# Kernel optimization log

Measured on AMD Instinct MI355X. Metric: run time of the kernel, lower is better.

The kernel has to match this reference:

```python
import jax, jax.numpy as jnp
import numpy as np

DIM = 192; HEADS = 6; WIN = 8; HIDDEN = int(DIM * 2.66); EPS = 1e-5

def dct_matrix(n):
    # DCT-II orthonormal matrix, matches get_dctMatrix(n, n)
    i = np.arange(n)[:, None]; j = np.arange(n)[None, :]
    M = np.cos(np.pi * i * (2 * j + 1) / (2 * n)) * np.sqrt(2.0 / n)
    M[0, :] = np.sqrt(1.0 / n)
    return jnp.asarray(M, dtype=jnp.float32)

def layernorm_c(x, w, b):
    # WithBias LayerNorm over channel dim of BCHW (restormer to_3d/to_4d style)
    mu = x.mean(axis=1, keepdims=True)
    var = ((x - mu) ** 2).mean(axis=1, keepdims=True)
    return (x - mu) / jnp.sqrt(var + EPS) * w[None, :, None, None] + b[None, :, None, None]

def conv1x1(x, w, b=None):
    y = jnp.einsum('oc,bchw->bohw', w, x)
    return y if b is None else y + b[None, :, None, None]

def dwconv3x3(x, w):
    return jax.lax.conv_general_dilated(x, w, (1, 1), ((1, 1), (1, 1)),
        dimension_numbers=('NCHW', 'OIHW', 'NCHW'), feature_group_count=x.shape[1])

def l2norm(x):
    n = jnp.sqrt(jnp.sum(x * x, axis=-1, keepdims=True))
    return x / jnp.maximum(n, 1e-12)

def window_channel_attn(qkv, temperature):
    # 'b (z head c) (h1 h) (w1 w) -> z (b h1 w1) head c (h w)'
    b, _, H, W = qkv.shape
    cph = DIM // HEADS
    h1, w1 = H // WIN, W // WIN
    t = qkv.reshape(b, 3, HEADS, cph, h1, WIN, w1, WIN)
    t = t.transpose(1, 0, 4, 6, 2, 3, 5, 7).reshape(3, b * h1 * w1, HEADS, cph, WIN * WIN)
    q, k, v = t[0], t[1], t[2]
    q = l2norm(q); k = l2norm(k)
    attn = jnp.einsum('nhce,nhde->nhcd', q, k) * temperature[None]  # channel x channel per window
    attn = jax.nn.softmax(attn, axis=-1)
    out = jnp.einsum('nhcd,nhde->nhce', attn, v)
    out = out.reshape(b, h1, w1, HEADS, cph, WIN, WIN)
    out = out.transpose(0, 3, 4, 1, 5, 2, 6).reshape(b, DIM, H, W)
    return out

def forward(x, norm1_w, norm1_b, w_qkv, w_dw, temperature, w_proj, b_proj,
            norm2_w, norm2_b, w_in, w_dwf, w_out):
    B, C, H, W = x.shape
    Mh = dct_matrix(H); Mw = dct_matrix(W)
    # attention branch in DCT domain
    y = layernorm_c(x, norm1_w, norm1_b)
    y = jnp.einsum('ph,bchw->bcpw', Mh, y)      # dct2dx: Mh @ y @ Mw.T
    y = jnp.einsum('bcpw,qw->bcpq', y, Mw)
    qkv = dwconv3x3(conv1x1(y, w_qkv), w_dw)
    a = window_channel_attn(qkv, temperature)
    a = conv1x1(a, w_proj, b_proj)
    a = jnp.einsum('bcpq,qw->bcpw', a, Mw)      # idct2dx: Mh.T @ a @ Mw
    a = jnp.einsum('bcpw,ph->bchw', a, Mh)
    x1 = x + a
    # gated-dconv FFN branch
    z = layernorm_c(x1, norm2_w, norm2_b)
    f = dwconv3x3(conv1x1(z, w_in), w_dwf)
    f1, f2 = jnp.split(f, 2, axis=1)
    f = jax.nn.gelu(f1, approximate=False) * f2
    f = conv1x1(f, w_out)
    return x1 + f

def setup_inputs() -> dict:
    key = jax.random.key(0)
    ks = jax.random.split(key, 8)
    B, C, H, W = 2, DIM, 192, 192
    s = 0.02
    return {
        'x': jax.random.normal(ks[0], (B, C, H, W), jnp.float32),
        'norm1_w': jnp.ones((C,), jnp.float32),
        'norm1_b': jnp.zeros((C,), jnp.float32),
        'w_qkv': jax.random.normal(ks[1], (3 * C, C), jnp.float32) * s,
        'w_dw': jax.random.normal(ks[2], (3 * C, 1, 3, 3), jnp.float32) * s,
        'temperature': jnp.ones((HEADS, 1, 1), jnp.float32) / np.float32(np.sqrt(C)),
        'w_proj': jax.random.normal(ks[3], (C, C), jnp.float32) * s,
        'b_proj': jnp.zeros((C,), jnp.float32),
        'norm2_w': jnp.ones((C,), jnp.float32),
        'norm2_b': jnp.zeros((C,), jnp.float32),
        'w_in': jax.random.normal(ks[4], (2 * HIDDEN, C), jnp.float32) * s,
        'w_dwf': jax.random.normal(ks[5], (2 * HIDDEN, 1, 3, 3), jnp.float32) * s,
        'w_out': jax.random.normal(ks[6], (C, HIDDEN), jnp.float32) * s,
    }

def reference(x, norm1_w, norm1_b, w_qkv, w_dw, temperature, w_proj, b_proj,
              norm2_w, norm2_b, w_in, w_dwf, w_out):
    return forward(x, norm1_w, norm1_b, w_qkv, w_dw, temperature, w_proj, b_proj,
                   norm2_w, norm2_b, w_in, w_dwf, w_out)
```

## Files before the change

kernel.cpp:

```cpp
#include <hip/hip_runtime.h>
#include <hip/hip_bf16.h>

typedef __hip_bfloat16 bft;
typedef __attribute__((ext_vector_type(8))) short bf16x8;
typedef __attribute__((ext_vector_type(4))) float f32x4;

#define BLK 256
static constexpr int Cc = 192;
static constexpr int L  = 192;
static constexpr int S  = 36864;
static constexpr int Bn = 2;
static constexpr int HID = 510;
static constexpr int CH = 64;
static constexpr int FTR = (CH + 2) * L;
static constexpr int GTR = CH * L;
static constexpr double PI_D = 3.141592653589793238462643383279502884;

__device__ __forceinline__ float ldf(const float* p) { return *p; }
__device__ __forceinline__ float ldf(const bft* p)   { return __bfloat162float(*p); }
__device__ __forceinline__ void  stf(float* p, float v) { *p = v; }
__device__ __forceinline__ void  stf(bft* p, float v)   { *p = __float2bfloat16(v); }
__device__ __forceinline__ unsigned short f2bfu(float f) {
    bft h = __float2bfloat16(f);
    return *reinterpret_cast<const unsigned short*>(&h);
}
__device__ __forceinline__ unsigned short bfu(const bft* p) {
    return *reinterpret_cast<const unsigned short*>(p);
}
__device__ __forceinline__ float bu2f(unsigned short u) {
    unsigned int x = (unsigned int)u << 16;
    return __uint_as_float(x);
}
__device__ __forceinline__ bf16x8 ld8(const unsigned short* p) {
    union { unsigned int u[4]; bf16x8 v; } t;
    const unsigned int* q = reinterpret_cast<const unsigned int*>(p);
    t.u[0] = q[0]; t.u[1] = q[1]; t.u[2] = q[2]; t.u[3] = q[3];
    return t.v;
}

__global__ __launch_bounds__(BLK) void k_dct_init(bft* __restrict__ dctb,
                                                  bft* __restrict__ dctTb) {
    int idx = blockIdx.x * BLK + threadIdx.x;
    if (idx >= L * L) return;
    int p = idx / L, h = idx - p * L;
    double v = (p == 0) ? sqrt(1.0 / L)
                        : cos(PI_D * p * (2 * h + 1) / (2.0 * L)) * sqrt(2.0 / L);
    bft bv = __float2bfloat16((float)v);
    dctb[p * L + h] = bv;
    dctTb[h * L + p] = bv;
}

__global__ __launch_bounds__(BLK) void k_cvt(const float* __restrict__ src,
                                             bft* __restrict__ dst,
                                             int Mr, int Kr, int Kp) {
    int idx = blockIdx.x * BLK + threadIdx.x;
    int m = idx / Kp, k = idx - m * Kp;
    float v = (m < Mr && k < Kr) ? src[(size_t)m * Kr + k] : 0.f;
    dst[idx] = __float2bfloat16(v);
}

__global__ __launch_bounds__(BLK) void k_cvt_ffn(const float* __restrict__ src,
                                                 bft* __restrict__ dst) {
    int idx = blockIdx.x * BLK + threadIdx.x;
    int m = idx / Cc, k = idx - m * Cc;
    float v = 0.f;
    if (m < 510) v = src[(size_t)m * Cc + k];
    else if (m >= 512 && m < 1022) v = src[(size_t)(m - 2) * Cc + k];
    dst[idx] = __float2bfloat16(v);
}

template <typename TI, bool TRANS>
__global__ __launch_bounds__(BLK) void k_lnt(const TI* __restrict__ x,
                                             const float* __restrict__ w,
                                             const float* __restrict__ b,
                                             bft* __restrict__ out,
                                             long zI, long zO) {
    __shared__ float t[192][65];
    __shared__ float mus[64], rs[64];
    const int tid = threadIdx.x;
    const int s0 = blockIdx.x * 64;
    const TI* xp = x + (size_t)blockIdx.y * zI;
    if constexpr (sizeof(TI) == 4) {
        for (int id = tid; id < 192 * 16; id += BLK) {
            int c = id >> 4, q = id & 15;
            float4 v = *reinterpret_cast<const float4*>(
                (const float*)xp + (size_t)c * S + s0 + q * 4);
            t[c][q * 4 + 0] = v.x; t[c][q * 4 + 1] = v.y;
            t[c][q * 4 + 2] = v.z; t[c][q * 4 + 3] = v.w;
        }
    } else {
        for (int id = tid; id < 192 * 8; id += BLK) {
            int c = id >> 3, q = id & 7;
            uint4 raw = *reinterpret_cast<const uint4*>(
                (const bft*)xp + (size_t)c * S + s0 + q * 8);
            const unsigned short* u = reinterpret_cast<const unsigned short*>(&raw);
#pragma unroll
            for (int e = 0; e < 8; ++e) t[c][q * 8 + e] = bu2f(u[e]);
        }
    }
    __syncthreads();
    {
        int px = tid >> 2, g = tid & 3;
        float sum = 0.f, sq = 0.f;
#pragma unroll
        for (int j = 0; j < 48; ++j) {
            float v = t[g * 48 + j][px];
            sum += v; sq += v * v;
        }
        sum += __shfl_xor(sum, 1); sum += __shfl_xor(sum, 2);
        sq  += __shfl_xor(sq, 1);  sq  += __shfl_xor(sq, 2);
        float mu = sum * (1.f / Cc);
        float var = sq * (1.f / Cc) - mu * mu;
        float r = rsqrtf(var + 1e-5f);
        if (g == 0) { mus[px] = mu; rs[px] = r; }
    }
    __syncthreads();
    bft* op = out + (size_t)blockIdx.y * zO;
    if constexpr (!TRANS) {
        for (int id = tid; id < 192 * 8; id += BLK) {
            int c = id >> 3, q = id & 7;
            float wc = w[c], bc = b[c];
            unsigned short v8[8];
#pragma unroll
            for (int e = 0; e < 8; ++e) {
                int px = q * 8 + e;
                v8[e] = f2bfu((t[c][px] - mus[px]) * rs[px] * wc + bc);
            }
            *reinterpret_cast<uint4*>(op + (size_t)c * S + s0 + q * 8) =
                *reinterpret_cast<uint4*>(v8);
        }
    } else {
#pragma unroll
        for (int qq = 0; qq < 3; ++qq) {
            for (int id = tid; id < 512; id += BLK) {
                int s = id >> 3, qlo = id & 7;
                int q = qq * 8 + qlo;
                float mu = mus[s], r = rs[s];
                unsigned short v8[8];
#pragma unroll
                for (int e = 0; e < 8; ++e) {
                    int c = q * 8 + e;
                    v8[e] = f2bfu((t[c][s] - mu) * r * w[c] + b[c]);
                }
                *reinterpret_cast<uint4*>(op + (size_t)(s0 + s) * Cc + q * 8) =
                    *reinterpret_cast<uint4*>(v8);
            }
        }
    }
}

__global__ __launch_bounds__(BLK) void k_tr(const bft* __restrict__ in,
                                            bft* __restrict__ out, long z) {
    __shared__ unsigned short t[32][72];
    const int tid = threadIdx.x;
    const int s0 = blockIdx.x * 64, c0 = blockIdx.y * 32;
    const bft* ip = in + (size_t)blockIdx.z * z;
    bft* op = out + (size_t)blockIdx.z * z;
    {
        int c = tid >> 3, sc = (tid & 7) * 8;
        *reinterpret_cast<uint4*>(&t[c][sc]) =
            *reinterpret_cast<const uint4*>(ip + (size_t)(c0 + c) * S + s0 + sc);
    }
    __syncthreads();
    {
        int s = tid >> 2, cc = (tid & 3) * 8;
        unsigned short v[8];
#pragma unroll
        for (int q = 0; q < 8; ++q) v[q] = t[cc + q][s];
        *reinterpret_cast<uint4*>(op + (size_t)(s0 + s) * Cc + c0 + cc) =
            *reinterpret_cast<uint4*>(v);
    }
}

__global__ __launch_bounds__(BLK) void k_w2s(const bft* __restrict__ src,
                                             bft* __restrict__ dst,
                                             long zI, long zO) {
    __shared__ unsigned short t[192][100];
    const int tid = threadIdx.x;
    const int hh = blockIdx.x;
    const int ch0 = blockIdx.y * 96;
    const int bz = blockIdx.z;
    const int h1 = hh >> 3, ii = hh & 7;
    const bft* ip = src + (size_t)bz * zI;
    for (int id = tid; id < 192 * 12; id += BLK) {
        int r = id / 12, q = id - r * 12;
        int w1 = r >> 3, jj = r & 7;
        int s = (h1 * 24 + w1) * 64 + ii * 8 + jj;
        *reinterpret_cast<uint4*>(&t[r][q * 8]) =
            *reinterpret_cast<const uint4*>(ip + (size_t)s * Cc + ch0 + q * 8);
    }
    __syncthreads();
    bft* op = dst + (size_t)bz * zO;
    for (int id = tid; id < 96 * 24; id += BLK) {
        int c = id / 24, q = id - c * 24;
        unsigned short v[8];
#pragma unroll
        for (int e = 0; e < 8; ++e) v[e] = t[q * 8 + e][c];
        *reinterpret_cast<uint4*>(op + (size_t)(ch0 + c) * S + (size_t)hh * L + q * 8) =
            *reinterpret_cast<uint4*>(v);
    }
}

template <int WR, int WC, int FM, int FN, int KSTEP, int BMODE, int OMODE,
          bool GSWAP, bool SWIZ, bool AMASK, bool HASBIAS, bool BIASN,
          bool HASRES, typename OutT, typename ResT>
__global__ __launch_bounds__(256) void k_mm(
    const bft* __restrict__ A, int strideA, int Mreal, long zA,
    const bft* __restrict__ B, int strideB, long zB,
    OutT* __restrict__ Out, int strideO, long zO,
    const float* __restrict__ bias,
    const ResT* __restrict__ Res, long zR,
    int K, int rlo, int rhi) {
    constexpr int BM = WR * FM * 16, BN = WC * FN * 16;
    constexpr int AV = KSTEP / 8;
    constexpr int KL = (BM + BN) * (KSTEP + 8);
    constexpr int RST = (OMODE == 3) ? BN * (BM + 8)
                      : (OMODE == 5 ? BM * (BN + 8) : 0);
    constexpr int LDSZ = (KL > RST) ? KL : RST;
    __shared__ unsigned short lds[LDSZ];
    unsigned short (*Al)[KSTEP + 8] =
        reinterpret_cast<unsigned short(*)[KSTEP + 8]>(lds);
    unsigned short (*Bl)[KSTEP + 8] =
        reinterpret_cast<unsigned short(*)[KSTEP + 8]>(lds + BM * (KSTEP + 8));
    const int tid = threadIdx.x;
    int bx = blockIdx.x, by = blockIdx.y;
    if constexpr (SWIZ) {
        int nbx = gridDim.x, nby = gridDim.y;
        int nwg = nbx * nby;
        int orig = bx + nbx * by;
        int cpx = nwg >> 3;
        int swz = (orig & 7) * cpx + (orig >> 3);
        bx = swz % nbx; by = swz / nbx;
    }
    const int n0 = (GSWAP ? by : bx) * BN;
    const int m0 = (GSWAP ? bx : by) * BM;
    const int bz = blockIdx.z;
    const int lane = tid & 63, wv = tid >> 6;
    const int wr = wv / WC, wc = wv % WC;
    const int l15 = lane & 15, l4 = lane >> 4;
    f32x4 acc[FM][FN] = {};

    const bft* Ab = A + (size_t)bz * zA;
    const bft* Bb = B + (size_t)bz * zB;

    for (int k0 = 0; k0 < K; k0 += KSTEP) {
        for (int id = tid; id < BM * AV; id += 256) {
            int row = id / AV, kc = (id % AV) * 8;
            int gm = m0 + row;
            if constexpr (AMASK) {
                uint4 val = make_uint4(0, 0, 0, 0);
                if (gm >= rlo && gm < rhi)
                    val = *reinterpret_cast<const uint4*>(
                        Ab + (size_t)gm * strideA + k0 + kc);
                *reinterpret_cast<uint4*>(&Al[row][kc]) = val;
            } else {
                if (gm >= Mreal) gm = Mreal - 1;
                *reinterpret_cast<uint4*>(&Al[row][kc]) =
                    *reinterpret_cast<const uint4*>(Ab + (size_t)gm * strideA + k0 + kc);
            }
        }
        for (int id = tid; id < BN * AV; id += 256) {
            int row = id / AV, kc = (id % AV) * 8;
            int gn = n0 + row;
            uint4 val;
            if constexpr (BMODE == 2) {
                val = *reinterpret_cast<const uint4*>(
                    Bb + (size_t)gn * strideB + k0 + kc);
            } else {
                if (gn >= rlo && gn < rhi)
                    val = *reinterpret_cast<const uint4*>(
                        Bb + (size_t)gn * strideB + k0 + kc);
                else
                    val = make_uint4(0, 0, 0, 0);
            }
            *reinterpret_cast<uint4*>(&Bl[row][kc]) = val;
        }
        __syncthreads();
#pragma unroll
        for (int kk = 0; kk < KSTEP / 32; ++kk) {
            bf16x8 af[FM], bf[FN];
#pragma unroll
            for (int i = 0; i < FM; ++i)
                af[i] = *reinterpret_cast<const bf16x8*>(
                    &Al[wr * FM * 16 + i * 16 + l15][kk * 32 + l4 * 8]);
#pragma unroll
            for (int j = 0; j < FN; ++j)
                bf[j] = *reinterpret_cast<const bf16x8*>(
                    &Bl[wc * FN * 16 + j * 16 + l15][kk * 32 + l4 * 8]);
#pragma unroll
            for (int i = 0; i < FM; ++i)
#pragma unroll
                for (int j = 0; j < FN; ++j)
                    acc[i][j] = __builtin_amdgcn_mfma_f32_16x16x32_bf16(
                        af[i], bf[j], acc[i][j], 0, 0, 0);
        }
        __syncthreads();
    }
    if constexpr (OMODE == 3) {
        constexpr int OST = BM + 8;
        unsigned short* Ol = lds;
#pragma unroll
        for (int i = 0; i < FM; ++i) {
            int mB = wr * FM * 16 + i * 16 + l4 * 4;
#pragma unroll
            for (int j = 0; j < FN; ++j) {
                int n = wc * FN * 16 + j * 16 + l15;
                unsigned short v[4];
#pragma unroll
                for (int r = 0; r < 4; ++r) v[r] = f2bfu(acc[i][j][r]);
                *reinterpret_cast<uint2*>(&Ol[n * OST + mB]) =
                    *reinterpret_cast<uint2*>(v);
            }
        }
        __syncthreads();
        constexpr int TPR = BM / 64;
        for (int row = tid / TPR; row < BN; row += 256 / TPR) {
            int seg = (tid % TPR) * 64;
            bft* dst = (bft*)Out + (size_t)bz * zO
                     + (size_t)(n0 + row) * strideO + m0 + seg;
            const unsigned short* src = &Ol[row * OST + seg];
#pragma unroll
            for (int q = 0; q < 8; ++q)
                *reinterpret_cast<uint4*>(dst + q * 8) =
                    *reinterpret_cast<const uint4*>(src + q * 8);
        }
        return;
    }
    if constexpr (OMODE == 5) {
        constexpr int OST = BN + 8;
        unsigned short* Ol = lds;
#pragma unroll
        for (int i = 0; i < FM; ++i) {
            int mB = wr * FM * 16 + i * 16 + l4 * 4;
#pragma unroll
            for (int j = 0; j < FN; ++j) {
                int n = wc * FN * 16 + j * 16 + l15;
#pragma unroll
                for (int r = 0; r < 4; ++r)
                    Ol[(mB + r) * OST + n] = f2bfu(acc[i][j][r]);
            }
        }
        __syncthreads();
        constexpr int TPR = BN / 64;
        for (int row = tid / TPR; row < BM; row += 256 / TPR) {
            if (m0 + row >= Mreal) continue;
            int seg = (tid % TPR) * 64;
            bft* dst = (bft*)Out + (size_t)bz * zO
                     + (size_t)(m0 + row) * strideO + n0 + seg;
            const unsigned short* src = &Ol[row * OST + seg];
#pragma unroll
            for (int q = 0; q < 8; ++q)
                *reinterpret_cast<uint4*>(dst + q * 8) =
                    *reinterpret_cast<const uint4*>(src + q * 8);
        }
        return;
    }
#pragma unroll
    for (int i = 0; i < FM; ++i) {
        int mB = m0 + wr * FM * 16 + i * 16 + l4 * 4;
#pragma unroll
        for (int j = 0; j < FN; ++j) {
            int n = n0 + wc * FN * 16 + j * 16 + l15;
#pragma unroll
            for (int r = 0; r < 4; ++r) {
                int m = mB + r;
                if (m >= Mreal) continue;
                float vv = acc[i][j][r];
                if constexpr (HASBIAS) vv += BIASN ? bias[n] : bias[m];
                size_t idx = (size_t)bz * zO + (size_t)m * strideO + n;
                if constexpr (HASRES)
                    vv += ldf(Res + (size_t)bz * zR + (size_t)m * strideO + n);
                stf(Out + idx, vv);
            }
        }
    }
}

__global__ __launch_bounds__(BLK) void k_dwconv(const bft* __restrict__ in,
                                                long inZ,
                                                const float* __restrict__ wt,
                                                bft* __restrict__ out,
                                                long outZ) {
    int t = blockIdx.x * BLK + threadIdx.x;
    int ch2 = t / (S / 8);
    int rem = t - ch2 * (S / 8);
    int b = ch2 / Cc, ch = ch2 - b * Cc;
    int h = rem / 24, wb = (rem - h * 24) * 8;
    const float* wp = wt + (size_t)ch * 9;
    const bft* ip = in + (size_t)b * inZ + (size_t)ch * S;
    float acc[8] = {};
#pragma unroll
    for (int dy = -1; dy <= 1; ++dy) {
        int hh = h + dy;
        if (hh < 0 || hh >= L) continue;
        const bft* rp = ip + hh * L + wb;
        float e[10];
        uint4 mid = *reinterpret_cast<const uint4*>(rp);
        const unsigned short* ms = reinterpret_cast<const unsigned short*>(&mid);
#pragma unroll
        for (int q = 0; q < 8; ++q) e[q + 1] = bu2f(ms[q]);
        e[0] = (wb > 0) ? ldf(rp - 1) : 0.f;
        e[9] = (wb + 8 < L) ? ldf(rp + 8) : 0.f;
        float c0 = wp[(dy + 1) * 3], c1 = wp[(dy + 1) * 3 + 1], c2 = wp[(dy + 1) * 3 + 2];
#pragma unroll
        for (int q = 0; q < 8; ++q)
            acc[q] += c0 * e[q] + c1 * e[q + 1] + c2 * e[q + 2];
    }
    int win = (h >> 3) * 24 + (wb >> 3);
    int e0 = (h & 7) * 8;
    unsigned short ov[8];
#pragma unroll
    for (int q = 0; q < 8; ++q) ov[q] = f2bfu(acc[q]);
    *reinterpret_cast<uint4*>(out + (size_t)b * outZ + (size_t)ch * S + win * 64 + e0) =
        *reinterpret_cast<uint4*>(ov);
}

__global__ __launch_bounds__(256) void k_attn_mfma(
    const bft* __restrict__ QW, long zQ,
    const bft* __restrict__ KW, long zK,
    const bft* __restrict__ VW, long zV,
    const float* __restrict__ temp,
    bft* __restrict__ outp, long zO) {
    __shared__ unsigned short qls[4][32 * 66];
    __shared__ unsigned short kls[4][32 * 66];
    __shared__ unsigned short vls[4][32 * 66];
    __shared__ float rqs[4][32], rks[4][32];
    const int tid = threadIdx.x;
    const int wv = tid >> 6, lane = tid & 63;
    const int win = blockIdx.x * 4 + wv;
    const int hd = blockIdx.y;
    const int bz = blockIdx.z;
    const int l15 = lane & 15, l4 = lane >> 4;
    unsigned short* ql = qls[wv];
    unsigned short* kl = kls[wv];
    unsigned short* vl = vls[wv];
    const size_t base = (size_t)(hd * 32) * S + (size_t)win * 64;

#pragma unroll
    for (int i = 0; i < 4; ++i) {
        int c = i * 8 + (lane >> 3), e0 = (lane & 7) * 8;
        size_t g = base + (size_t)c * S + e0;
        uint4 vq = *reinterpret_cast<const uint4*>(QW + (size_t)bz * zQ + g);
        uint4 vk = *reinterpret_cast<const uint4*>(KW + (size_t)bz * zK + g);
        uint4 vvv = *reinterpret_cast<const uint4*>(VW + (size_t)bz * zV + g);
        unsigned int* dq = reinterpret_cast<unsigned int*>(&ql[c * 66 + e0]);
        unsigned int* dk = reinterpret_cast<unsigned int*>(&kl[c * 66 + e0]);
        unsigned int* dv = reinterpret_cast<unsigned int*>(&vl[c * 66 + e0]);
        dq[0] = vq.x; dq[1] = vq.y; dq[2] = vq.z; dq[3] = vq.w;
        dk[0] = vk.x; dk[1] = vk.y; dk[2] = vk.z; dk[3] = vk.w;
        dv[0] = vvv.x; dv[1] = vvv.y; dv[2] = vvv.z; dv[3] = vvv.w;
    }
    __syncthreads();
    {
        int row = lane & 31;
        const unsigned short* src = (lane < 32) ? ql : kl;
        float s = 0.f;
#pragma unroll
        for (int w = 0; w < 32; ++w) {
            unsigned int d = *reinterpret_cast<const unsigned int*>(&src[row * 66 + 2 * w]);
            float a = bu2f((unsigned short)(d & 0xffff));
            float b = bu2f((unsigned short)(d >> 16));
            s += a * a + b * b;
        }
        float r = 1.f / fmaxf(sqrtf(s), 1e-12f);
        if (lane < 32) rqs[wv][row] = r; else rks[wv][row] = r;
    }
    __syncthreads();
    f32x4 at[2][2] = {};
#pragma unroll
    for (int ks = 0; ks < 2; ++ks) {
        bf16x8 aq[2], bk[2];
#pragma unroll
        for (int i = 0; i < 2; ++i)
            aq[i] = ld8(&ql[(i * 16 + l15) * 66 + ks * 32 + l4 * 8]);
#pragma unroll
        for (int j = 0; j < 2; ++j)
            bk[j] = ld8(&kl[(j * 16 + l15) * 66 + ks * 32 + l4 * 8]);
#pragma unroll
        for (int i = 0; i < 2; ++i)
#pragma unroll
            for (int j = 0; j < 2; ++j)
                at[i][j] = __builtin_amdgcn_mfma_f32_16x16x32_bf16(
                    aq[i], bk[j], at[i][j], 0, 0, 0);
    }
    float tpr = temp[hd];
    float rk0 = rks[wv][l15] * tpr, rk1 = rks[wv][16 + l15] * tpr;
    float pr[2][2][4];
#pragma unroll
    for (int i = 0; i < 2; ++i)
#pragma unroll
        for (int r = 0; r < 4; ++r) {
            int c = i * 16 + l4 * 4 + r;
            float rq = rqs[wv][c];
            float v0 = at[i][0][r] * rq * rk0;
            float v1 = at[i][1][r] * rq * rk1;
            float mx = fmaxf(v0, v1);
#pragma unroll
            for (int m = 1; m < 16; m <<= 1) mx = fmaxf(mx, __shfl_xor(mx, m));
            v0 = __expf(v0 - mx);
            v1 = __expf(v1 - mx);
            float sm = v0 + v1;
#pragma unroll
            for (int m = 1; m < 16; m <<= 1) sm += __shfl_xor(sm, m);
            float inv = 1.f / sm;
            pr[i][0][r] = v0 * inv;
            pr[i][1][r] = v1 * inv;
        }
    __syncthreads();
    unsigned short* pl = ql;
#pragma unroll
    for (int i = 0; i < 2; ++i)
#pragma unroll
        for (int j = 0; j < 2; ++j)
#pragma unroll
            for (int r = 0; r < 4; ++r)
                pl[(i * 16 + l4 * 4 + r) * 34 + j * 16 + l15] = f2bfu(pr[i][j][r]);
    __syncthreads();
    bf16x8 ap[2];
#pragma unroll
    for (int i = 0; i < 2; ++i)
        ap[i] = ld8(&pl[(i * 16 + l15) * 34 + l4 * 8]);
    f32x4 o[2][4] = {};
#pragma unroll
    for (int j = 0; j < 4; ++j) {
        unsigned short tv[8];
#pragma unroll
        for (int q = 0; q < 8; ++q)
            tv[q] = vl[(l4 * 8 + q) * 66 + j * 16 + l15];
        bf16x8 bv = *reinterpret_cast<bf16x8*>(tv);
#pragma unroll
        for (int i = 0; i < 2; ++i)
            o[i][j] = __builtin_amdgcn_mfma_f32_16x16x32_bf16(ap[i], bv, o[i][j], 0, 0, 0);
    }
#pragma unroll
    for (int i = 0; i < 2; ++i)
#pragma unroll
        for (int j = 0; j < 4; ++j) {
            int e = j * 16 + l15, cl = i * 16 + l4 * 4;
            unsigned short v[4];
#pragma unroll
            for (int r = 0; r < 4; ++r) v[r] = f2bfu(o[i][j][r]);
            unsigned short* row = ((e < 32) ? kl : vl) + (e & 31) * 40 + cl;
            *reinterpret_cast<uint2*>(row) = *reinterpret_cast<uint2*>(v);
        }
    {
        const unsigned short* row = ((lane < 32) ? kl : vl) + (lane & 31) * 40;
        bft* dst = outp + (size_t)bz * zO + (size_t)(win * 64 + lane) * Cc + hd * 32;
#pragma unroll
        for (int q = 0; q < 4; ++q)
            *reinterpret_cast<uint4*>(dst + q * 8) =
                *reinterpret_cast<const uint4*>(row + q * 8);
    }
}

__global__ __launch_bounds__(BLK) void k_gateT(const bft* __restrict__ fTg,
                                               const float* __restrict__ wt,
                                               bft* __restrict__ gTg) {
    __shared__ float w1s[64][9];
    __shared__ float w2s[64][9];
    const int tid = threadIdx.x;
    const int cbase = blockIdx.y * 64;
    const bft* fT = fTg + (size_t)blockIdx.z * FTR * 1024;
    bft* gT = gTg + (size_t)blockIdx.z * GTR * 512;
    for (int id = tid; id < 576; id += BLK) {
        int cl = id / 9, k = id - cl * 9;
        int c = cbase + cl;
        w1s[cl][k] = (c < HID) ? wt[(size_t)c * 9 + k] : 0.f;
        w2s[cl][k] = (c < HID) ? wt[(size_t)(c + HID) * 9 + k] : 0.f;
    }
    __syncthreads();
    int px = blockIdx.x * 32 + (tid >> 3);
    int cgl = (tid & 7) * 8;
    int hc = px / L, w = px - hc * L;
    float a1[8] = {}, a2[8] = {};
#pragma unroll
    for (int dy = 0; dy < 3; ++dy) {
#pragma unroll
        for (int dx = 0; dx < 3; ++dx) {
            int ww = w + dx - 1;
            if (ww < 0 || ww >= L) continue;
            size_t frow = (size_t)((hc + dy) * L + ww) * 1024 + cbase + cgl;
            uint4 u1 = *reinterpret_cast<const uint4*>(fT + frow);
            uint4 u2 = *reinterpret_cast<const uint4*>(fT + frow + 512);
            const unsigned short* e1 = reinterpret_cast<const unsigned short*>(&u1);
            const unsigned short* e2 = reinterpret_cast<const unsigned short*>(&u2);
            int k = dy * 3 + dx;
#pragma unroll
            for (int j = 0; j < 8; ++j) {
                a1[j] += w1s[cgl + j][k] * bu2f(e1[j]);
                a2[j] += w2s[cgl + j][k] * bu2f(e2[j]);
            }
        }
    }
    unsigned short ov[8];
#pragma unroll
    for (int j = 0; j < 8; ++j) {
        float ge = 0.5f * a1[j] * (1.f + erff(a1[j] * 0.70710678118654752f));
        ov[j] = f2bfu(ge * a2[j]);
    }
    *reinterpret_cast<uint4*>(gT + (size_t)px * 512 + cbase + cgl) =
        *reinterpret_cast<uint4*>(ov);
}

extern "C" void kernel_launch(void* const* d_in, const int* in_sizes, int n_in,
                              void* d_out, int out_size, void* d_ws, size_t ws_size,
                              hipStream_t stream) {
    const float* x      = (const float*)d_in[0];
    const float* n1w    = (const float*)d_in[1];
    const float* n1b    = (const float*)d_in[2];
    const float* w_qkv  = (const float*)d_in[3];
    const float* w_dw   = (const float*)d_in[4];
    const float* temp   = (const float*)d_in[5];
    const float* w_proj = (const float*)d_in[6];
    const float* b_proj = (const float*)d_in[7];
    const float* n2w    = (const float*)d_in[8];
    const float* n2b    = (const float*)d_in[9];
    const float* w_in   = (const float*)d_in[10];
    const float* w_dwf  = (const float*)d_in[11];
    const float* w_out  = (const float*)d_in[12];
    float* outp = (float*)d_out;

    const long CS = (long)Cc * S;
    const size_t DCT_B = 147456;
    const size_t BUF_B = (size_t)Bn * CS * 2;
    const size_t QKV_B = (size_t)Bn * 3 * CS * 2;
    const size_t WB_B  = 884736;
    const size_t NEED  = DCT_B + 3 * BUF_B + QKV_B + WB_B;
    if (ws_size < NEED) return;

    char* p = (char*)d_ws;
    bft* dctb  = (bft*)p;
    bft* dctTb = dctb + L * L;
    p += DCT_B;
    bft* X1    = (bft*)p;                  p += BUF_B;
    bft* PbB   = (bft*)p;                  p += BUF_B;
    bft* QbB   = (bft*)p;                  p += BUF_B;
    bft* QKV   = (bft*)p;                  p += QKV_B;
    bft* w_qkv_b = (bft*)p;
    bft* w_proj_b = w_qkv_b + 576 * 192;
    bft* w_in_b  = w_proj_b + 192 * 192;
    bft* w_out_b = w_in_b + 1024 * 192;
    bft* fT = QKV;
    bft* gT = QKV + (size_t)Bn * FTR * 1024;
    bft* attnT = QKV + CS;

    k_dct_init<<<144, BLK, 0, stream>>>(dctb, dctTb);
    k_cvt<<<432, BLK, 0, stream>>>(w_qkv, w_qkv_b, 576, 192, 192);
    k_cvt<<<144, BLK, 0, stream>>>(w_proj, w_proj_b, 192, 192, 192);
    k_cvt_ffn<<<768, BLK, 0, stream>>>(w_in, w_in_b);
    k_cvt<<<384, BLK, 0, stream>>>(w_out, w_out_b, 192, 510, 512);

    k_lnt<float, false><<<dim3(S / 64, Bn), BLK, 0, stream>>>(x, n1w, n1b, PbB, CS, CS);
    k_mm<2, 2, 2, 6, 64, 2, 3, false, false, false, false, false, false, bft, float><<<dim3(1, 3, Bn * Cc), 256, 0, stream>>>(
        PbB, L, L, S,  dctb, L, 0,  QbB, L, S,  nullptr, nullptr, 0,  L, 0, 0);
    k_mm<2, 2, 2, 6, 64, 2, 3, false, false, false, false, false, false, bft, float><<<dim3(1, 3, Bn * Cc), 256, 0, stream>>>(
        QbB, L, L, S,  dctb, L, 0,  PbB, L, S,  nullptr, nullptr, 0,  L, 0, 0);
    k_tr<<<dim3(576, 6, Bn), BLK, 0, stream>>>(PbB, QbB, CS);
    k_mm<2, 2, 4, 4, 64, 2, 5, true, true, false, false, false, false, bft, float><<<dim3(5, 288, Bn), 256, 0, stream>>>(
        w_qkv_b, Cc, 576, 0,  QbB, Cc, CS,  QKV, S, 3 * CS,  nullptr, nullptr, 0,  Cc, 0, 0);
    k_dwconv<<<6912, BLK, 0, stream>>>(QKV, 3 * CS, w_dw, PbB, CS);
    k_dwconv<<<6912, BLK, 0, stream>>>(QKV + CS, 3 * CS, w_dw + Cc * 9, QbB, CS);
    k_dwconv<<<6912, BLK, 0, stream>>>(QKV + 2 * CS, 3 * CS, w_dw + 2 * Cc * 9, QKV, 3 * CS);
    k_attn_mfma<<<dim3(144, 6, Bn), 256, 0, stream>>>(
        PbB, CS, QbB, CS, QKV, 3 * CS, temp, attnT, 3 * CS);
    k_mm<2, 2, 2, 6, 64, 2, 0, false, false, false, true, true, false, bft, float><<<dim3(1, 576, Bn), 256, 0, stream>>>(
        attnT, Cc, S, 3 * CS,  w_proj_b, Cc, 0,  PbB, Cc, CS,  b_proj, (const float*)nullptr, 0,  Cc, 0, 0);
    k_w2s<<<dim3(192, 2, Bn), BLK, 0, stream>>>(PbB, QbB, CS, CS);
    k_mm<2, 2, 2, 6, 64, 2, 3, false, false, false, false, false, false, bft, float><<<dim3(1, 3, Bn * Cc), 256, 0, stream>>>(
        QbB, L, L, S,  dctTb, L, 0,  PbB, L, S,  nullptr, nullptr, 0,  L, 0, 0);
    k_mm<2, 2, 2, 6, 64, 2, 0, false, false, false, false, false, true, bft, float><<<dim3(1, 3, Bn * Cc), 256, 0, stream>>>(
        dctTb, L, L, 0,  PbB, L, S,  X1, L, S,  nullptr, x, S,  L, 0, 0);

    k_lnt<bft, true><<<dim3(S / 64, Bn), BLK, 0, stream>>>(X1, n2w, n2b, QbB, CS, CS);
    for (int ck = 0; ck < 3; ++ck) {
        int h0 = ck * CH;
        long off = (long)(h0 - 1) * L;
        int rlo = (h0 == 0) ? L : 0;
        int rhi = (h0 == 2 * CH) ? (FTR - L) : FTR;
        k_mm<2, 2, 4, 4, 64, 4, 3, true, true, true, false, false, false, bft, float><<<dim3(8, 99, Bn), 256, 0, stream>>>(
            w_in_b, Cc, 1024, 0,  QbB + off * Cc, Cc, CS,  fT, 1024, (long)FTR * 1024,
            nullptr, nullptr, 0,  Cc, rlo, rhi);
        k_gateT<<<dim3(GTR / 32, 8, Bn), BLK, 0, stream>>>(fT, w_dwf, gT);
        k_mm<2, 2, 2, 4, 64, 2, 0, true, true, true, false, false, true, float, bft><<<dim3(3, 96, Bn), 256, 0, stream>>>(
            w_out_b, 512, 192, 0,  gT, 512, (long)GTR * 512,
            outp + (size_t)h0 * L, S, CS,
            nullptr, X1 + (size_t)h0 * L, CS,  512, 0, 0);
    }
}
```

Before: 744.3 us.

## Merge q/k/v depthwise convs into one launch and halve FFN chunk count

Replaces the three per-tensor depthwise-conv launches with a single kernel that dispatches on z to separate q, k and v output buffers, adding a dedicated V buffer. The FFN is split into two chunks of 96 rows instead of three of 64, with gT moved to its own workspace region so it no longer aliases the QKV scratch. A template flag in the FFN matmuls is also flipped. Fewer launches and larger grids are meant to cut launch overhead and tail effects, at the cost of more workspace and a larger fT footprint inside the QKV buffer.

New measurement: 737.2 us. No clear change (-1.0%).

```diff
diff --git a/kernel.cpp b/kernel.cpp
--- a/kernel.cpp
+++ b/kernel.cpp
@@ -11,9 +11,9 @@
 static constexpr int S  = 36864;
 static constexpr int Bn = 2;
 static constexpr int HID = 510;
-static constexpr int CH = 64;
-static constexpr int FTR = (CH + 2) * L;
-static constexpr int GTR = CH * L;
+static constexpr int CH2 = 96;
+static constexpr int FTR2 = (CH2 + 2) * L;
+static constexpr int GTR2 = CH2 * L;
 static constexpr double PI_D = 3.141592653589793238462643383279502884;
 
 __device__ __forceinline__ float ldf(const float* p) { return *p; }
@@ -376,18 +376,21 @@
     }
 }
 
-__global__ __launch_bounds__(BLK) void k_dwconv(const bft* __restrict__ in,
-                                                long inZ,
-                                                const float* __restrict__ wt,
-                                                bft* __restrict__ out,
-                                                long outZ) {
+__global__ __launch_bounds__(BLK) void k_dwconv3(const bft* __restrict__ qkv,
+                                                 const float* __restrict__ wt,
+                                                 bft* __restrict__ q_out,
+                                                 bft* __restrict__ k_out,
+                                                 bft* __restrict__ v_out,
+                                                 long CSl) {
     int t = blockIdx.x * BLK + threadIdx.x;
-    int ch2 = t / (S / 8);
-    int rem = t - ch2 * (S / 8);
-    int b = ch2 / Cc, ch = ch2 - b * Cc;
+    int ch3 = t / (S / 8);
+    int rem = t - ch3 * (S / 8);
+    int b = ch3 / 576, zc = ch3 - b * 576;
+    int z = zc / Cc, ch = zc - z * Cc;
     int h = rem / 24, wb = (rem - h * 24) * 8;
-    const float* wp = wt + (size_t)ch * 9;
-    const bft* ip = in + (size_t)b * inZ + (size_t)ch * S;
+    const float* wp = wt + (size_t)zc * 9;
+    const bft* ip = qkv + (size_t)b * 3 * CSl + (size_t)zc * S;
+    bft* base = (z == 0) ? q_out : (z == 1) ? k_out : v_out;
     float acc[8] = {};
 #pragma unroll
     for (int dy = -1; dy <= 1; ++dy) {
@@ -411,7 +414,7 @@
     unsigned short ov[8];
 #pragma unroll
     for (int q = 0; q < 8; ++q) ov[q] = f2bfu(acc[q]);
-    *reinterpret_cast<uint4*>(out + (size_t)b * outZ + (size_t)ch * S + win * 64 + e0) =
+    *reinterpret_cast<uint4*>(base + (size_t)b * CSl + (size_t)ch * S + win * 64 + e0) =
         *reinterpret_cast<uint4*>(ov);
 }
 
@@ -560,8 +563,8 @@
     __shared__ float w2s[64][9];
     const int tid = threadIdx.x;
     const int cbase = blockIdx.y * 64;
-    const bft* fT = fTg + (size_t)blockIdx.z * FTR * 1024;
-    bft* gT = gTg + (size_t)blockIdx.z * GTR * 512;
+    const bft* fT = fTg + (size_t)blockIdx.z * FTR2 * 1024;
+    bft* gT = gTg + (size_t)blockIdx.z * GTR2 * 512;
     for (int id = tid; id < 576; id += BLK) {
         int cl = id / 9, k = id - cl * 9;
         int c = cbase + cl;
@@ -625,7 +628,8 @@
     const size_t BUF_B = (size_t)Bn * CS * 2;
     const size_t QKV_B = (size_t)Bn * 3 * CS * 2;
     const size_t WB_B  = 884736;
-    const size_t NEED  = DCT_B + 3 * BUF_B + QKV_B + WB_B;
+    const size_t GT_B  = (size_t)Bn * GTR2 * 512 * 2;
+    const size_t NEED  = DCT_B + 4 * BUF_B + QKV_B + WB_B + GT_B;
     if (ws_size < NEED) return;
 
     char* p = (char*)d_ws;
@@ -635,13 +639,15 @@
     bft* X1    = (bft*)p;                  p += BUF_B;
     bft* PbB   = (bft*)p;                  p += BUF_B;
     bft* QbB   = (bft*)p;                  p += BUF_B;
+    bft* VW    = (bft*)p;                  p += BUF_B;
     bft* QKV   = (bft*)p;                  p += QKV_B;
     bft* w_qkv_b = (bft*)p;
     bft* w_proj_b = w_qkv_b + 576 * 192;
     bft* w_in_b  = w_proj_b + 192 * 192;
     bft* w_out_b = w_in_b + 1024 * 192;
+    p += WB_B;
+    bft* gT = (bft*)p;
     bft* fT = QKV;
-    bft* gT = QKV + (size_t)Bn * FTR * 1024;
     bft* attnT = QKV + CS;
 
     k_dct_init<<<144, BLK, 0, stream>>>(dctb, dctTb);
@@ -658,11 +664,9 @@
     k_tr<<<dim3(576, 6, Bn), BLK, 0, stream>>>(PbB, QbB, CS);
     k_mm<2, 2, 4, 4, 64, 2, 5, true, true, false, false, false, false, bft, float><<<dim3(5, 288, Bn), 256, 0, stream>>>(
         w_qkv_b, Cc, 576, 0,  QbB, Cc, CS,  QKV, S, 3 * CS,  nullptr, nullptr, 0,  Cc, 0, 0);
-    k_dwconv<<<6912, BLK, 0, stream>>>(QKV, 3 * CS, w_dw, PbB, CS);
-    k_dwconv<<<6912, BLK, 0, stream>>>(QKV + CS, 3 * CS, w_dw + Cc * 9, QbB, CS);
-    k_dwconv<<<6912, BLK, 0, stream>>>(QKV + 2 * CS, 3 * CS, w_dw + 2 * Cc * 9, QKV, 3 * CS);
+    k_dwconv3<<<20736, BLK, 0, stream>>>(QKV, w_dw, PbB, QbB, VW, CS);
     k_attn_mfma<<<dim3(144, 6, Bn), 256, 0, stream>>>(
-        PbB, CS, QbB, CS, QKV, 3 * CS, temp, attnT, 3 * CS);
+        PbB, CS, QbB, CS, VW, CS, temp, attnT, 3 * CS);
     k_mm<2, 2, 2, 6, 64, 2, 0, false, false, false, true, true, false, bft, float><<<dim3(1, 576, Bn), 256, 0, stream>>>(
         attnT, Cc, S, 3 * CS,  w_proj_b, Cc, 0,  PbB, Cc, CS,  b_proj, (const float*)nullptr, 0,  Cc, 0, 0);
     k_w2s<<<dim3(192, 2, Bn), BLK, 0, stream>>>(PbB, QbB, CS, CS);
@@ -672,18 +676,18 @@
         dctTb, L, L, 0,  PbB, L, S,  X1, L, S,  nullptr, x, S,  L, 0, 0);
 
     k_lnt<bft, true><<<dim3(S / 64, Bn), BLK, 0, stream>>>(X1, n2w, n2b, QbB, CS, CS);
-    for (int ck = 0; ck < 3; ++ck) {
-        int h0 = ck * CH;
+    for (int ck = 0; ck < 2; ++ck) {
+        int h0 = ck * CH2;
         long off = (long)(h0 - 1) * L;
-        int rlo = (h0 == 0) ? L : 0;
-        int rhi = (h0 == 2 * CH) ? (FTR - L) : FTR;
-        k_mm<2, 2, 4, 4, 64, 4, 3, true, true, true, false, false, false, bft, float><<<dim3(8, 99, Bn), 256, 0, stream>>>(
-            w_in_b, Cc, 1024, 0,  QbB + off * Cc, Cc, CS,  fT, 1024, (long)FTR * 1024,
+        int rlo = (ck == 0) ? L : 0;
+        int rhi = (ck == 1) ? (FTR2 - L) : FTR2;
+        k_mm<2, 2, 4, 4, 64, 4, 3, true, true, false, false, false, false, bft, float><<<dim3(8, 147, Bn), 256, 0, stream>>>(
+            w_in_b, Cc, 1024, 0,  QbB + off * Cc, Cc, CS,  fT, 1024, (long)FTR2 * 1024,
             nullptr, nullptr, 0,  Cc, rlo, rhi);
-        k_gateT<<<dim3(GTR / 32, 8, Bn), BLK, 0, stream>>>(fT, w_dwf, gT);
-        k_mm<2, 2, 2, 4, 64, 2, 0, true, true, true, false, false, true, float, bft><<<dim3(3, 96, Bn), 256, 0, stream>>>(
-            w_out_b, 512, 192, 0,  gT, 512, (long)GTR * 512,
-            outp + (size_t)h0 * L, S, CS,
-            nullptr, X1 + (size_t)h0 * L, CS,  512, 0, 0);
-    }
-}
+        k_gateT<<<dim3(GTR2 / 32, 8, Bn), BLK, 0, stream>>>(fT, w_dwf, gT);
+        k_mm<2, 2, 2, 4, 64, 2, 0, true, true, false, false, false, true, float, bft><<<dim3(3, 144, Bn), 256, 0, stream>>>(
+            w_out_b, 512, 192, 0,  gT, 512, (long)GTR2 * 512,
+            outp + (size_t)ck * GTR2, S, CS,
+            nullptr, X1 + (size_t)ck * GTR2, CS,  512, 0, 0);
+    }
+}
```
